# Kernel tuning notes

Hardware: AMD Instinct MI355X
Metric: run time of the kernel (lower is better)

The kernel has to match this reference:

```python
import jax, jax.numpy as jnp
import numpy as np

B, N, D, D_MODEL = 4, 2048, 512, 512


def setup_inputs() -> dict:
    key = jax.random.key(0)
    kx, kq, kk, kv, ks = jax.random.split(key, 5)
    scale = 1.0 / np.sqrt(D)
    x = jax.random.normal(kx, (B, N, D), dtype=jnp.float32)
    Wq = (jax.random.normal(kq, (D, D_MODEL), dtype=jnp.float32) * scale)
    Wk = (jax.random.normal(kk, (D, D_MODEL), dtype=jnp.float32) * scale)
    Wv = (jax.random.normal(kv, (D, D_MODEL), dtype=jnp.float32) * scale)
    Ws = (jax.random.normal(ks, (D, 1), dtype=jnp.float32) * scale)
    return {"x": x, "Wq": Wq, "Wk": Wk, "Wv": Wv, "Ws": Ws}


def reference(x, Wq, Wk, Wv, Ws):
    # Projections (Linear, no bias)
    Q = x @ Wq                      # (B, N, d_model)
    K = x @ Wk                      # (B, N, d_model)
    V = x @ Wv                      # (B, N, d_model)
    sigma = x @ Ws                  # (B, N, 1)

    n = x.shape[1]
    dm = Wq.shape[1]

    # Prior association: Gaussian kernel over |i-j| distance, row-normalized
    idx = jnp.arange(n)
    dist = jnp.abs(idx[:, None] - idx[None, :]).astype(x.dtype)      # (N, N)
    inv_norm = 1.0 / (jnp.sqrt(2.0 * jnp.pi).astype(x.dtype) * jnp.abs(sigma))
    gaussian = inv_norm * jnp.exp(-0.5 * jnp.square(dist[None] / sigma))  # (B,N,N)
    P = gaussian / jnp.sum(gaussian, axis=-1, keepdims=True)

    # Series association: scaled dot-product softmax attention
    scores = jnp.einsum('bnd,bmd->bnm', Q, K) / jnp.sqrt(jnp.asarray(dm, x.dtype))
    S = jax.nn.softmax(scores, axis=-1)                               # (B,N,N)

    # Reconstruction
    Z = S @ V                                                          # (B,N,d_model)
    return (Z, P)
```

## Files before the change

### kernel.cpp

```cpp
#include <hip/hip_runtime.h>

typedef float f32x4 __attribute__((ext_vector_type(4)));
typedef short s16x8 __attribute__((ext_vector_type(8)));
typedef unsigned short us4 __attribute__((ext_vector_type(4)));

#define MFMA16(a, b, c) __builtin_amdgcn_mfma_f32_16x16x32_bf16(a, b, c, 0, 0, 0)

#define GLOAD_LDS16(gp, lp) __builtin_amdgcn_global_load_lds( \
    (__attribute__((address_space(1))) void*)(gp),            \
    (__attribute__((address_space(3))) void*)(lp), 16, 0, 0)

__device__ __forceinline__ unsigned short f2bf(float f) {
    union { float f; unsigned u; } v; v.f = f;
    unsigned r = v.u + 0x7fffu + ((v.u >> 16) & 1u);
    return (unsigned short)(r >> 16);
}

__device__ __forceinline__ void gemm_core128(
    const unsigned short* __restrict__ Ab, size_t Astride,
    const unsigned short* __restrict__ Bb, size_t Bstride,
    int K, unsigned short* As, unsigned short* Bs,
    int t, f32x4 acc[4][4])
{
    const int wave = t >> 6, lane = t & 63;
    const int c = lane & 15, quad = lane >> 4;
    const int wm = (wave >> 1) * 64, wn = (wave & 1) * 64;
    const int srow = t >> 2;
    const int scol = (t & 3) * 8;

    for (int k0 = 0; k0 < K; k0 += 32) {
        __syncthreads();
        const unsigned short* ga = Ab + (size_t)srow * Astride + k0 + scol;
        const unsigned short* gb = Bb + (size_t)srow * Bstride + k0 + scol;
        GLOAD_LDS16(ga,                 As + t * 8);
        GLOAD_LDS16(ga + 64 * Astride,  As + 2048 + t * 8);
        GLOAD_LDS16(gb,                 Bs + t * 8);
        GLOAD_LDS16(gb + 64 * Bstride,  Bs + 2048 + t * 8);
        __syncthreads();

        s16x8 af[4], bf[4];
        #pragma unroll
        for (int i = 0; i < 4; i++)
            af[i] = *(const s16x8*)(As + (wm + i * 16 + c) * 32 + quad * 8);
        #pragma unroll
        for (int i = 0; i < 4; i++)
            bf[i] = *(const s16x8*)(Bs + (wn + i * 16 + c) * 32 + quad * 8);
        #pragma unroll
        for (int mt = 0; mt < 4; mt++)
            #pragma unroll
            for (int nt = 0; nt < 4; nt++)
                acc[mt][nt] = MFMA16(af[mt], bf[nt], acc[mt][nt]);
    }
}

__global__ __launch_bounds__(256) void k_convert(
    const float* __restrict__ x, const float* __restrict__ wq,
    const float* __restrict__ wk, const float* __restrict__ wv,
    unsigned short* __restrict__ xbf, unsigned short* __restrict__ wt,
    float* __restrict__ lg)
{
    __shared__ __align__(16) unsigned short lt[64][72];

    int bid = blockIdx.x, t = threadIdx.x;
    if (bid < 4096) {
        int gid = bid * 256 + t;
        float4 v = ((const float4*)x)[gid];
        us4 o = { f2bf(v.x), f2bf(v.y), f2bf(v.z), f2bf(v.w) };
        ((us4*)xbf)[gid] = o;
    } else if (bid < 4288) {
        int idx = bid - 4096;
        int w = idx >> 6;
        int tile = idx & 63;
        int tk = tile >> 3, tn = tile & 7;
        const float* src = ((w == 0) ? wq : (w == 1) ? wk : wv)
                         + (size_t)(tk * 64) * 512 + tn * 64;

        int row = t >> 2;
        int c0 = (t & 3) * 16;
        const float4* s = (const float4*)(src + (size_t)row * 512 + c0);
        #pragma unroll
        for (int q = 0; q < 4; q++) {
            float4 v = s[q];
            lt[c0 + q * 4 + 0][row] = f2bf(v.x);
            lt[c0 + q * 4 + 1][row] = f2bf(v.y);
            lt[c0 + q * 4 + 2][row] = f2bf(v.z);
            lt[c0 + q * 4 + 3][row] = f2bf(v.w);
        }
        __syncthreads();

        int n = t >> 2;
        int k0 = (t & 3) * 16;
        s16x8 a = *(const s16x8*)&lt[n][k0];
        s16x8 b = *(const s16x8*)&lt[n][k0 + 8];
        unsigned short* dst = wt + (((size_t)(w * 512 + tn * 64 + n)) << 9)
                                 + tk * 64 + k0;
        *(s16x8*)dst = a;
        *(s16x8*)(dst + 8) = b;
    } else {
        lg[(bid - 4288) * 256 + t] = 0.f;
    }
}

__global__ __launch_bounds__(256) void k_proj(
    const unsigned short* __restrict__ xbf, const unsigned short* __restrict__ wt,
    unsigned short* __restrict__ qbf, unsigned short* __restrict__ kbf,
    unsigned short* __restrict__ vtbf)
{
    __shared__ __align__(16) unsigned short As[128 * 32];
    __shared__ __align__(16) unsigned short Bs[128 * 32];

    int t = threadIdx.x;
    int m0 = blockIdx.x * 128, n0 = blockIdx.y * 128;
    f32x4 acc[4][4] = {};

    gemm_core128(xbf + (size_t)m0 * 512, 512, wt + (size_t)n0 * 512, 512,
                 512, As, Bs, t, acc);

    int wave = t >> 6, lane = t & 63, c = lane & 15, quad = lane >> 4;
    int wm = (wave >> 1) * 64, wn = (wave & 1) * 64;
    int sel = blockIdx.y >> 2;

    if (sel < 2) {
        unsigned short* dst = sel ? kbf : qbf;
        int ncol0 = n0 - sel * 512;
        #pragma unroll
        for (int mt = 0; mt < 4; mt++) {
            #pragma unroll
            for (int nt = 0; nt < 4; nt++) {
                int col = ncol0 + wn + nt * 16 + c;
                #pragma unroll
                for (int r = 0; r < 4; r++) {
                    int rw = m0 + wm + mt * 16 + quad * 4 + r;
                    dst[(size_t)rw * 512 + col] = f2bf(acc[mt][nt][r]);
                }
            }
        }
    } else {
        #pragma unroll
        for (int mt = 0; mt < 4; mt++) {
            int rw0 = m0 + wm + mt * 16 + quad * 4;
            int bb = rw0 >> 11, nn = rw0 & 2047;
            #pragma unroll
            for (int nt = 0; nt < 4; nt++) {
                int d = (n0 - 1024) + wn + nt * 16 + c;
                us4 pk = { f2bf(acc[mt][nt][0]), f2bf(acc[mt][nt][1]),
                           f2bf(acc[mt][nt][2]), f2bf(acc[mt][nt][3]) };
                *(us4*)(vtbf + ((size_t)(bb * 512 + d)) * 2048 + nn) = pk;
            }
        }
    }
}

__device__ __forceinline__ void score_body(
    const unsigned short* __restrict__ qbf, const unsigned short* __restrict__ kbf,
    unsigned short* __restrict__ pbf, float* __restrict__ lg,
    int b, int m0, int n0, int t, unsigned short* As, unsigned short* Bs)
{
    f32x4 acc[4][4] = {};
    gemm_core128(qbf + (size_t)(b * 2048 + m0) * 512, 512,
                 kbf + (size_t)(b * 2048 + n0) * 512, 512,
                 512, As, Bs, t, acc);

    int wave = t >> 6, lane = t & 63, c = lane & 15, quad = lane >> 4;
    int wm = (wave >> 1) * 64, wn = (wave & 1) * 64;
    const float scale = 0.044194173824159216f;

    #pragma unroll
    for (int mt = 0; mt < 4; mt++) {
        #pragma unroll
        for (int r = 0; r < 4; r++) {
            int row = m0 + wm + mt * 16 + quad * 4 + r;
            float rs = 0.f;
            #pragma unroll
            for (int nt = 0; nt < 4; nt++) {
                float p = __expf(acc[mt][nt][r] * scale);
                rs += p;
                pbf[(size_t)(b * 2048 + row) * 2048 + n0 + wn + nt * 16 + c] = f2bf(p);
            }
            rs += __shfl_xor(rs, 1, 16);
            rs += __shfl_xor(rs, 2, 16);
            rs += __shfl_xor(rs, 4, 16);
            rs += __shfl_xor(rs, 8, 16);
            if (c == 0) atomicAdd(&lg[b * 2048 + row], rs);
        }
    }
}

__device__ __forceinline__ void prior_wave(
    const float* __restrict__ x, const float* __restrict__ wsv,
    float* __restrict__ pout, int row, int lane)
{
    const float4* xr = (const float4*)(x + (size_t)row * 512);
    const float4* wr = (const float4*)wsv;
    float4 a0 = xr[lane * 2],     b0 = wr[lane * 2];
    float4 a1 = xr[lane * 2 + 1], b1 = wr[lane * 2 + 1];
    float part = a0.x * b0.x + a0.y * b0.y + a0.z * b0.z + a0.w * b0.w
               + a1.x * b1.x + a1.y * b1.y + a1.z * b1.z + a1.w * b1.w;
    #pragma unroll
    for (int o = 32; o; o >>= 1) part += __shfl_xor(part, o, 64);
    float sigma = part;
    float inv2 = 0.5f / (sigma * sigma);

    int i = row & 2047;
    float g[32];
    float sum = 0.f;
    #pragma unroll
    for (int u = 0; u < 8; u++) {
        #pragma unroll
        for (int v = 0; v < 4; v++) {
            float d = (float)(u * 256 + lane * 4 + v - i);
            float e = __expf(-(d * d) * inv2);
            g[u * 4 + v] = e;
            sum += e;
        }
    }
    #pragma unroll
    for (int o = 32; o; o >>= 1) sum += __shfl_xor(sum, o, 64);
    float inv = 1.0f / sum;

    float4* pr = (float4*)(pout + (size_t)row * 2048);
    #pragma unroll
    for (int u = 0; u < 8; u++) {
        float4 o4 = { g[u * 4] * inv, g[u * 4 + 1] * inv,
                      g[u * 4 + 2] * inv, g[u * 4 + 3] * inv };
        pr[u * 64 + lane] = o4;
    }
}

__global__ __launch_bounds__(256) void k_score_prior(
    const unsigned short* __restrict__ qbf, const unsigned short* __restrict__ kbf,
    unsigned short* __restrict__ pbf, float* __restrict__ lg,
    const float* __restrict__ x, const float* __restrict__ wsv,
    float* __restrict__ pout)
{
    __shared__ __align__(16) unsigned short As[128 * 32];
    __shared__ __align__(16) unsigned short Bs[128 * 32];

    int bid = blockIdx.x, t = threadIdx.x;
    if (bid < 1024) {
        int b = bid >> 8, r = bid & 255;
        score_body(qbf, kbf, pbf, lg, b, (r & 15) * 128, (r >> 4) * 128, t, As, Bs);
    } else {
        int row = (bid - 1024) * 4 + (t >> 6);
        prior_wave(x, wsv, pout, row, t & 63);
    }
}

__global__ __launch_bounds__(256) void k_score(
    const unsigned short* __restrict__ qbf, const unsigned short* __restrict__ kbf,
    unsigned short* __restrict__ pbf, float* __restrict__ lg)
{
    __shared__ __align__(16) unsigned short As[128 * 32];
    __shared__ __align__(16) unsigned short Bs[128 * 32];
    score_body(qbf, kbf, pbf, lg, blockIdx.z,
               blockIdx.x * 128, blockIdx.y * 128, threadIdx.x, As, Bs);
}

__global__ __launch_bounds__(256) void k_out(
    const unsigned short* __restrict__ pbf, const unsigned short* __restrict__ vtbf,
    const float* __restrict__ lg, float* __restrict__ zout)
{
    __shared__ __align__(16) unsigned short As[128 * 32];
    __shared__ __align__(16) unsigned short Bs[64 * 32];
    __shared__ float invl[128];

    int t = threadIdx.x;
    int b = blockIdx.z;
    int m0 = blockIdx.x * 128, n0 = blockIdx.y * 64;

    if (t < 128) invl[t] = 1.0f / lg[b * 2048 + m0 + t];

    const unsigned short* Ab = pbf + (size_t)(b * 2048 + m0) * 2048;
    const unsigned short* Bb = vtbf + (size_t)(b * 512 + n0) * 2048;

    const int wave = t >> 6, lane = t & 63;
    const int c = lane & 15, quad = lane >> 4;
    const int wm = (wave >> 1) * 64, wn = (wave & 1) * 32;
    const int srow = t >> 2;
    const int scol = (t & 3) * 8;

    f32x4 acc[4][2] = {};

    for (int k0 = 0; k0 < 2048; k0 += 32) {
        __syncthreads();
        const unsigned short* ga = Ab + (size_t)srow * 2048 + k0 + scol;
        GLOAD_LDS16(ga,             As + t * 8);
        GLOAD_LDS16(ga + 64 * 2048, As + 2048 + t * 8);
        GLOAD_LDS16(Bb + (size_t)srow * 2048 + k0 + scol, Bs + t * 8);
        __syncthreads();

        s16x8 af[4], bf[2];
        #pragma unroll
        for (int i = 0; i < 4; i++)
            af[i] = *(const s16x8*)(As + (wm + i * 16 + c) * 32 + quad * 8);
        #pragma unroll
        for (int i = 0; i < 2; i++)
            bf[i] = *(const s16x8*)(Bs + (wn + i * 16 + c) * 32 + quad * 8);
        #pragma unroll
        for (int mt = 0; mt < 4; mt++)
            #pragma unroll
            for (int nt = 0; nt < 2; nt++)
                acc[mt][nt] = MFMA16(af[mt], bf[nt], acc[mt][nt]);
    }

    #pragma unroll
    for (int mt = 0; mt < 4; mt++) {
        #pragma unroll
        for (int nt = 0; nt < 2; nt++) {
            #pragma unroll
            for (int r = 0; r < 4; r++) {
                int row = wm + mt * 16 + quad * 4 + r;
                zout[(size_t)(b * 2048 + m0 + row) * 512 + n0 + wn + nt * 16 + c]
                    = acc[mt][nt][r] * invl[row];
            }
        }
    }
}

__global__ __launch_bounds__(256) void k_prior(
    const float* __restrict__ x, const float* __restrict__ wsv,
    float* __restrict__ pout)
{
    int row = blockIdx.x * 4 + (threadIdx.x >> 6);
    prior_wave(x, wsv, pout, row, threadIdx.x & 63);
}

extern "C" void kernel_launch(void* const* d_in, const int* in_sizes, int n_in,
                              void* d_out, int out_size, void* d_ws, size_t ws_size,
                              hipStream_t stream)
{
    const float* x  = (const float*)d_in[0];
    const float* wq = (const float*)d_in[1];
    const float* wk = (const float*)d_in[2];
    const float* wv = (const float*)d_in[3];
    const float* ws = (const float*)d_in[4];

    float* zout = (float*)d_out;
    float* pout = zout + (size_t)4 * 2048 * 512;

    const size_t need = ((size_t)4194304 + 786432 + 3 * 4194304 + 16777216) * 2
                        + 8192 * 4;

    if (ws_size >= need) {
        unsigned short* base = (unsigned short*)d_ws;
        unsigned short* xbf  = base;
        unsigned short* wt   = xbf  + (size_t)4194304;
        unsigned short* qbf  = wt   + (size_t)786432;
        unsigned short* kbf  = qbf  + (size_t)4194304;
        unsigned short* vtbf = kbf  + (size_t)4194304;
        unsigned short* pbf  = vtbf + (size_t)4194304;
        float*          lg   = (float*)(pbf + (size_t)16777216);

        k_convert<<<dim3(4320), dim3(256), 0, stream>>>(x, wq, wk, wv, xbf, wt, lg);
        k_proj       <<<dim3(64, 12),   dim3(256), 0, stream>>>(xbf, wt, qbf, kbf, vtbf);
        k_score_prior<<<dim3(3072),     dim3(256), 0, stream>>>(qbf, kbf, pbf, lg, x, ws, pout);
        k_out        <<<dim3(16, 8, 4), dim3(256), 0, stream>>>(pbf, vtbf, lg, zout);
    } else {
        unsigned short* base = (unsigned short*)pout;
        unsigned short* pbf  = base;
        unsigned short* qbf  = base + (size_t)16777216;
        unsigned short* kbf  = qbf  + (size_t)4194304;
        unsigned short* vtbf = kbf  + (size_t)4194304;
        float*          lg   = (float*)(vtbf + (size_t)4194304);
        unsigned short* xbf  = base;
        unsigned short* wt   = base + (size_t)4194304;

        k_convert<<<dim3(4320), dim3(256), 0, stream>>>(x, wq, wk, wv, xbf, wt, lg);
        k_proj  <<<dim3(64, 12),    dim3(256), 0, stream>>>(xbf, wt, qbf, kbf, vtbf);
        k_score <<<dim3(16, 16, 4), dim3(256), 0, stream>>>(qbf, kbf, pbf, lg);
        k_out   <<<dim3(16, 8, 4),  dim3(256), 0, stream>>>(pbf, vtbf, lg, zout);
        k_prior <<<dim3(2048),      dim3(256), 0, stream>>>(x, ws, pout);
    }
}
```

Before: 200.1 us.

## Stage GEMM epilogues through LDS and compute softmax row sums via MFMA

The projection and score kernels now write their bf16 results into a padded shared-memory tile, then copy full rows to global memory with 16-byte vector stores, replacing scattered 2-byte stores. The softmax denominator is no longer built with shuffle reductions and float atomics. It is computed in the output GEMM by an extra MFMA against a vector of ones, which removes the lg buffer, its zeroing and the atomic traffic. In exchange each block adds a shared-memory round trip, extra barriers and a larger LDS footprint, plus extra MFMA work in k_out. The denominator is now summed from the bf16-rounded probabilities rather than the fp32 values.

```diff
diff --git a/kernel.cpp b/kernel.cpp
--- a/kernel.cpp
+++ b/kernel.cpp
@@ -15,6 +15,9 @@
     unsigned r = v.u + 0x7fffu + ((v.u >> 16) & 1u);
     return (unsigned short)(r >> 16);
 }
+
+#define RP 136
+#define SH128 (128 * RP)
 
 __device__ __forceinline__ void gemm_core128(
     const unsigned short* __restrict__ Ab, size_t Astride,
@@ -56,8 +59,7 @@
 __global__ __launch_bounds__(256) void k_convert(
     const float* __restrict__ x, const float* __restrict__ wq,
     const float* __restrict__ wk, const float* __restrict__ wv,
-    unsigned short* __restrict__ xbf, unsigned short* __restrict__ wt,
-    float* __restrict__ lg)
+    unsigned short* __restrict__ xbf, unsigned short* __restrict__ wt)
 {
     __shared__ __align__(16) unsigned short lt[64][72];
 
@@ -67,7 +69,7 @@
         float4 v = ((const float4*)x)[gid];
         us4 o = { f2bf(v.x), f2bf(v.y), f2bf(v.z), f2bf(v.w) };
         ((us4*)xbf)[gid] = o;
-    } else if (bid < 4288) {
+    } else {
         int idx = bid - 4096;
         int w = idx >> 6;
         int tile = idx & 63;
@@ -96,8 +98,6 @@
                                  + tk * 64 + k0;
         *(s16x8*)dst = a;
         *(s16x8*)(dst + 8) = b;
-    } else {
-        lg[(bid - 4288) * 256 + t] = 0.f;
     }
 }
 
@@ -106,15 +106,15 @@
     unsigned short* __restrict__ qbf, unsigned short* __restrict__ kbf,
     unsigned short* __restrict__ vtbf)
 {
-    __shared__ __align__(16) unsigned short As[128 * 32];
-    __shared__ __align__(16) unsigned short Bs[128 * 32];
+    __shared__ __align__(16) unsigned short sh[SH128];
 
     int t = threadIdx.x;
     int m0 = blockIdx.x * 128, n0 = blockIdx.y * 128;
     f32x4 acc[4][4] = {};
 
     gemm_core128(xbf + (size_t)m0 * 512, 512, wt + (size_t)n0 * 512, 512,
-                 512, As, Bs, t, acc);
+                 512, sh, sh + 4096, t, acc);
+    __syncthreads();
 
     int wave = t >> 6, lane = t & 63, c = lane & 15, quad = lane >> 4;
     int wm = (wave >> 1) * 64, wn = (wave & 1) * 64;
@@ -124,42 +124,56 @@
         unsigned short* dst = sel ? kbf : qbf;
         int ncol0 = n0 - sel * 512;
         #pragma unroll
-        for (int mt = 0; mt < 4; mt++) {
-            #pragma unroll
-            for (int nt = 0; nt < 4; nt++) {
-                int col = ncol0 + wn + nt * 16 + c;
+        for (int mt = 0; mt < 4; mt++)
+            #pragma unroll
+            for (int nt = 0; nt < 4; nt++)
                 #pragma unroll
-                for (int r = 0; r < 4; r++) {
-                    int rw = m0 + wm + mt * 16 + quad * 4 + r;
-                    dst[(size_t)rw * 512 + col] = f2bf(acc[mt][nt][r]);
-                }
-            }
-        }
+                for (int r = 0; r < 4; r++)
+                    sh[(wm + mt * 16 + quad * 4 + r) * RP + wn + nt * 16 + c]
+                        = f2bf(acc[mt][nt][r]);
+        __syncthreads();
+        int rr = t >> 1, hh = (t & 1) * 64;
+        const s16x8* sp = (const s16x8*)(sh + rr * RP + hh);
+        s16x8* dp = (s16x8*)(dst + (size_t)(m0 + rr) * 512 + ncol0 + hh);
+        s16x8 v[8];
+        #pragma unroll
+        for (int i = 0; i < 8; i++) v[i] = sp[i];
+        #pragma unroll
+        for (int i = 0; i < 8; i++) dp[i] = v[i];
     } else {
         #pragma unroll
-        for (int mt = 0; mt < 4; mt++) {
-            int rw0 = m0 + wm + mt * 16 + quad * 4;
-            int bb = rw0 >> 11, nn = rw0 & 2047;
-            #pragma unroll
-            for (int nt = 0; nt < 4; nt++) {
-                int d = (n0 - 1024) + wn + nt * 16 + c;
-                us4 pk = { f2bf(acc[mt][nt][0]), f2bf(acc[mt][nt][1]),
-                           f2bf(acc[mt][nt][2]), f2bf(acc[mt][nt][3]) };
-                *(us4*)(vtbf + ((size_t)(bb * 512 + d)) * 2048 + nn) = pk;
-            }
-        }
+        for (int mt = 0; mt < 4; mt++)
+            #pragma unroll
+            for (int nt = 0; nt < 4; nt++)
+                #pragma unroll
+                for (int r = 0; r < 4; r++)
+                    sh[(wn + nt * 16 + c) * RP + wm + mt * 16 + quad * 4 + r]
+                        = f2bf(acc[mt][nt][r]);
+        __syncthreads();
+        int bb = m0 >> 11, nn0 = m0 & 2047;
+        int dbase = n0 - 1024;
+        int dl = t >> 1, nh = (t & 1) * 64;
+        const s16x8* sp = (const s16x8*)(sh + dl * RP + nh);
+        s16x8* dp = (s16x8*)(vtbf + ((size_t)(bb * 512 + dbase + dl)) * 2048
+                                  + nn0 + nh);
+        s16x8 v[8];
+        #pragma unroll
+        for (int i = 0; i < 8; i++) v[i] = sp[i];
+        #pragma unroll
+        for (int i = 0; i < 8; i++) dp[i] = v[i];
     }
 }
 
 __device__ __forceinline__ void score_body(
     const unsigned short* __restrict__ qbf, const unsigned short* __restrict__ kbf,
-    unsigned short* __restrict__ pbf, float* __restrict__ lg,
-    int b, int m0, int n0, int t, unsigned short* As, unsigned short* Bs)
+    unsigned short* __restrict__ pbf,
+    int b, int m0, int n0, int t, unsigned short* sh)
 {
     f32x4 acc[4][4] = {};
     gemm_core128(qbf + (size_t)(b * 2048 + m0) * 512, 512,
                  kbf + (size_t)(b * 2048 + n0) * 512, 512,
-                 512, As, Bs, t, acc);
+                 512, sh, sh + 4096, t, acc);
+    __syncthreads();
 
     int wave = t >> 6, lane = t & 63, c = lane & 15, quad = lane >> 4;
     int wm = (wave >> 1) * 64, wn = (wave & 1) * 64;
@@ -169,21 +183,23 @@
     for (int mt = 0; mt < 4; mt++) {
         #pragma unroll
         for (int r = 0; r < 4; r++) {
-            int row = m0 + wm + mt * 16 + quad * 4 + r;
-            float rs = 0.f;
+            int row = wm + mt * 16 + quad * 4 + r;
             #pragma unroll
             for (int nt = 0; nt < 4; nt++) {
                 float p = __expf(acc[mt][nt][r] * scale);
-                rs += p;
-                pbf[(size_t)(b * 2048 + row) * 2048 + n0 + wn + nt * 16 + c] = f2bf(p);
+                sh[row * RP + wn + nt * 16 + c] = f2bf(p);
             }
-            rs += __shfl_xor(rs, 1, 16);
-            rs += __shfl_xor(rs, 2, 16);
-            rs += __shfl_xor(rs, 4, 16);
-            rs += __shfl_xor(rs, 8, 16);
-            if (c == 0) atomicAdd(&lg[b * 2048 + row], rs);
-        }
-    }
+        }
+    }
+    __syncthreads();
+    int rr = t >> 1, hh = (t & 1) * 64;
+    const s16x8* sp = (const s16x8*)(sh + rr * RP + hh);
+    s16x8* dp = (s16x8*)(pbf + (size_t)(b * 2048 + m0 + rr) * 2048 + n0 + hh);
+    s16x8 v[8];
+    #pragma unroll
+    for (int i = 0; i < 8; i++) v[i] = sp[i];
+    #pragma unroll
+    for (int i = 0; i < 8; i++) dp[i] = v[i];
 }
 
 __device__ __forceinline__ void prior_wave(
@@ -229,17 +245,16 @@
 
 __global__ __launch_bounds__(256) void k_score_prior(
     const unsigned short* __restrict__ qbf, const unsigned short* __restrict__ kbf,
-    unsigned short* __restrict__ pbf, float* __restrict__ lg,
+    unsigned short* __restrict__ pbf,
     const float* __restrict__ x, const float* __restrict__ wsv,
     float* __restrict__ pout)
 {
-    __shared__ __align__(16) unsigned short As[128 * 32];
-    __shared__ __align__(16) unsigned short Bs[128 * 32];
+    __shared__ __align__(16) unsigned short sh[SH128];
 
     int bid = blockIdx.x, t = threadIdx.x;
     if (bid < 1024) {
         int b = bid >> 8, r = bid & 255;
-        score_body(qbf, kbf, pbf, lg, b, (r & 15) * 128, (r >> 4) * 128, t, As, Bs);
+        score_body(qbf, kbf, pbf, b, (r & 15) * 128, (r >> 4) * 128, t, sh);
     } else {
         int row = (bid - 1024) * 4 + (t >> 6);
         prior_wave(x, wsv, pout, row, t & 63);
@@ -248,30 +263,23 @@
 
 __global__ __launch_bounds__(256) void k_score(
     const unsigned short* __restrict__ qbf, const unsigned short* __restrict__ kbf,
-    unsigned short* __restrict__ pbf, float* __restrict__ lg)
-{
-    __shared__ __align__(16) unsigned short As[128 * 32];
-    __shared__ __align__(16) unsigned short Bs[128 * 32];
-    score_body(qbf, kbf, pbf, lg, blockIdx.z,
-               blockIdx.x * 128, blockIdx.y * 128, threadIdx.x, As, Bs);
+    unsigned short* __restrict__ pbf)
+{
+    __shared__ __align__(16) unsigned short sh[SH128];
+    score_body(qbf, kbf, pbf, blockIdx.z,
+               blockIdx.x * 128, blockIdx.y * 128, threadIdx.x, sh);
 }
 
 __global__ __launch_bounds__(256) void k_out(
     const unsigned short* __restrict__ pbf, const unsigned short* __restrict__ vtbf,
-    const float* __restrict__ lg, float* __restrict__ zout)
+    float* __restrict__ zout)
 {
     __shared__ __align__(16) unsigned short As[128 * 32];
     __shared__ __align__(16) unsigned short Bs[64 * 32];
-    __shared__ float invl[128];
 
     int t = threadIdx.x;
     int b = blockIdx.z;
     int m0 = blockIdx.x * 128, n0 = blockIdx.y * 64;
-
-    if (t < 128) invl[t] = 1.0f / lg[b * 2048 + m0 + t];
-
-    const unsigned short* Ab = pbf + (size_t)(b * 2048 + m0) * 2048;
-    const unsigned short* Bb = vtbf + (size_t)(b * 512 + n0) * 2048;
 
     const int wave = t >> 6, lane = t & 63;
     const int c = lane & 15, quad = lane >> 4;
@@ -279,7 +287,15 @@
     const int srow = t >> 2;
     const int scol = (t & 3) * 8;
 
+    const unsigned short* Ab = pbf + (size_t)(b * 2048 + m0) * 2048;
+    const unsigned short* Bb = vtbf + (size_t)(b * 512 + n0) * 2048;
+
+    s16x8 ones;
+    #pragma unroll
+    for (int i = 0; i < 8; i++) ones[i] = (short)0x3F80;
+
     f32x4 acc[4][2] = {};
+    f32x4 accl[4] = {};
 
     for (int k0 = 0; k0 < 2048; k0 += 32) {
         __syncthreads();
@@ -297,21 +313,24 @@
         for (int i = 0; i < 2; i++)
             bf[i] = *(const s16x8*)(Bs + (wn + i * 16 + c) * 32 + quad * 8);
         #pragma unroll
-        for (int mt = 0; mt < 4; mt++)
+        for (int mt = 0; mt < 4; mt++) {
             #pragma unroll
             for (int nt = 0; nt < 2; nt++)
                 acc[mt][nt] = MFMA16(af[mt], bf[nt], acc[mt][nt]);
+            accl[mt] = MFMA16(af[mt], ones, accl[mt]);
+        }
     }
 
     #pragma unroll
     for (int mt = 0; mt < 4; mt++) {
         #pragma unroll
-        for (int nt = 0; nt < 2; nt++) {
-            #pragma unroll
-            for (int r = 0; r < 4; r++) {
-                int row = wm + mt * 16 + quad * 4 + r;
+        for (int r = 0; r < 4; r++) {
+            int row = wm + mt * 16 + quad * 4 + r;
+            float inv = 1.0f / accl[mt][r];
+            #pragma unroll
+            for (int nt = 0; nt < 2; nt++) {
                 zout[(size_t)(b * 2048 + m0 + row) * 512 + n0 + wn + nt * 16 + c]
-                    = acc[mt][nt][r] * invl[row];
+                    = acc[mt][nt][r] * inv;
             }
         }
     }
@@ -338,8 +357,7 @@
     float* zout = (float*)d_out;
     float* pout = zout + (size_t)4 * 2048 * 512;
 
-    const size_t need = ((size_t)4194304 + 786432 + 3 * 4194304 + 16777216) * 2
-                        + 8192 * 4;
+    const size_t need = ((size_t)4194304 + 786432 + 3 * 4194304 + 16777216) * 2;
 
     if (ws_size >= need) {
         unsigned short* base = (unsigned short*)d_ws;
@@ -349,26 +367,24 @@
         unsigned short* kbf  = qbf  + (size_t)4194304;
         unsigned short* vtbf = kbf  + (size_t)4194304;
         unsigned short* pbf  = vtbf + (size_t)4194304;
-        float*          lg   = (float*)(pbf + (size_t)16777216);
-
-        k_convert<<<dim3(4320), dim3(256), 0, stream>>>(x, wq, wk, wv, xbf, wt, lg);
+
+        k_convert<<<dim3(4288), dim3(256), 0, stream>>>(x, wq, wk, wv, xbf, wt);
         k_proj       <<<dim3(64, 12),   dim3(256), 0, stream>>>(xbf, wt, qbf, kbf, vtbf);
-        k_score_prior<<<dim3(3072),     dim3(256), 0, stream>>>(qbf, kbf, pbf, lg, x, ws, pout);
-        k_out        <<<dim3(16, 8, 4), dim3(256), 0, stream>>>(pbf, vtbf, lg, zout);
+        k_score_prior<<<dim3(3072),     dim3(256), 0, stream>>>(qbf, kbf, pbf, x, ws, pout);
+        k_out        <<<dim3(16, 8, 4), dim3(256), 0, stream>>>(pbf, vtbf, zout);
     } else {
         unsigned short* base = (unsigned short*)pout;
         unsigned short* pbf  = base;
         unsigned short* qbf  = base + (size_t)16777216;
         unsigned short* kbf  = qbf  + (size_t)4194304;
         unsigned short* vtbf = kbf  + (size_t)4194304;
-        float*          lg   = (float*)(vtbf + (size_t)4194304);
         unsigned short* xbf  = base;
         unsigned short* wt   = base + (size_t)4194304;
 
-        k_convert<<<dim3(4320), dim3(256), 0, stream>>>(x, wq, wk, wv, xbf, wt, lg);
+        k_convert<<<dim3(4288), dim3(256), 0, stream>>>(x, wq, wk, wv, xbf, wt);
         k_proj  <<<dim3(64, 12),    dim3(256), 0, stream>>>(xbf, wt, qbf, kbf, vtbf);
-        k_score <<<dim3(16, 16, 4), dim3(256), 0, stream>>>(qbf, kbf, pbf, lg);
-        k_out   <<<dim3(16, 8, 4),  dim3(256), 0, stream>>>(pbf, vtbf, lg, zout);
+        k_score <<<dim3(16, 16, 4), dim3(256), 0, stream>>>(qbf, kbf, pbf);
+        k_out   <<<dim3(16, 8, 4),  dim3(256), 0, stream>>>(pbf, vtbf, zout);
         k_prior <<<dim3(2048),      dim3(256), 0, stream>>>(x, ws, pout);
     }
 }
```

Result: slower. 206.4 us (+3.1%).
